# Optimization experiments

Measured on AMD Instinct MI355X. Metric: run time of the kernel, lower is better.

## Reference

```python
import jax, jax.numpy as jnp
import numpy as np

B, DZ, DY, DX = 2, 200, 200, 100   # batch, voxel grid
N = 200000                          # active input voxels
C_IN, C_MID, C_OUT = 16, 64, 32
K = 27                              # 3x3x3 kernel offsets
EPS = 1e-5


def _pad_per_k(kid, a_in, a_out, pad_in, pad_out):
    # pack ragged per-offset pair lists into dense [K, Pmax] with dummy padding
    counts = np.bincount(kid, minlength=K)
    P = int(counts.max())
    I = np.full((K, P), pad_in, np.int32)
    O = np.full((K, P), pad_out, np.int32)
    order = np.argsort(kid, kind='stable')
    ks = kid[order]
    starts = np.cumsum(counts) - counts
    pos = np.arange(kid.size) - starts[ks]
    I[ks, pos] = a_in[order]
    O[ks, pos] = a_out[order]
    return I, O


def _build_structure(seed=0):
    # spconv-style indice-pair generation (rulebook) in numpy
    rng = np.random.default_rng(seed)
    lin = rng.choice(B * DZ * DY * DX, size=N, replace=False)
    b, r = np.divmod(lin, DZ * DY * DX)
    z, r = np.divmod(r, DY * DX)
    y, x = np.divmod(r, DX)
    coords = np.stack([b, z, y, x], 1)
    offs = np.stack(np.meshgrid(*[np.arange(3)] * 3, indexing='ij'), -1).reshape(K, 3)
    od = np.array([(DZ - 3) // 2 + 1, (DY - 3) // 2 + 1, (DX - 3) // 2 + 1])
    # stage 1: SparseConv3d k=3 s=2 p=0 -> output site o iff i = 2*o + k
    oc = coords[:, None, 1:] - offs[None]            # (N, 27, 3)
    valid = (oc >= 0).all(-1) & (oc % 2 == 0).all(-1)
    oq = oc // 2
    valid &= (oq < od).all(-1)
    pi, pk = np.nonzero(valid)
    oz, oy, ox = oq[pi, pk, 0], oq[pi, pk, 1], oq[pi, pk, 2]
    olin = ((coords[pi, 0] * od[0] + oz) * od[1] + oy) * od[2] + ox
    uniq, inv = np.unique(olin, return_inverse=True)
    n1 = int(len(uniq))
    p1_in, p1_out = _pad_per_k(pk, pi.astype(np.int32), inv.astype(np.int32), N, n1)
    # stage 2: SubMConv3d k=3 on stage-1 sites (output sites == input sites)
    c1b, r = np.divmod(uniq, od[0] * od[1] * od[2])
    c1z, r = np.divmod(r, od[1] * od[2])
    c1y, c1x = np.divmod(r, od[2])
    coords1 = np.stack([c1b, c1z, c1y, c1x], 1)
    nc = coords1[:, None, 1:] + (offs - 1)[None]     # (n1, 27, 3) neighbor coords
    valid2 = (nc >= 0).all(-1) & (nc < od).all(-1)
    pj, pk2 = np.nonzero(valid2)
    nl = ((coords1[pj, 0] * od[0] + nc[pj, pk2, 0]) * od[1] + nc[pj, pk2, 1]) * od[2] + nc[pj, pk2, 2]
    pos = np.minimum(np.searchsorted(uniq, nl), n1 - 1)
    ok = uniq[pos] == nl
    p2_in, p2_out = _pad_per_k(pk2[ok], pos[ok].astype(np.int32), pj[ok].astype(np.int32), n1, n1)
    return p1_in, p1_out, p2_in, p2_out, n1


def _ggs(feats, W, pin, pout, n_out):
    # gather-gemm-scatter sparse conv; pin padded with feats.shape[0], pout with n_out
    fpad = jnp.concatenate([feats, jnp.zeros((1, feats.shape[1]), feats.dtype)], 0)
    out = jnp.zeros((n_out + 1, W.shape[2]), feats.dtype)
    for k in range(W.shape[0]):
        out = out.at[pout[k]].add(fpad[pin[k]] @ W[k])
    return out[:n_out]


def _bn_relu(x, g, b):
    # BatchNorm1d (training-mode batch stats, biased var) + ReLU
    m = x.mean(0)
    v = x.var(0)
    return jax.nn.relu((x - m) * jax.lax.rsqrt(v + EPS) * g + b)


def setup_inputs():
    p1_in, p1_out, p2_in, p2_out, n1 = _build_structure(0)
    key = jax.random.key(0)
    k1, k2, k3, k4 = jax.random.split(key, 4)
    return {
        'feats': jax.random.normal(k1, (N, C_IN), jnp.float32),
        'W1': jax.random.normal(k2, (K, C_IN, C_MID), jnp.float32) * 0.05,
        'gamma1': jnp.ones((C_MID,), jnp.float32),
        'beta1': jnp.zeros((C_MID,), jnp.float32),
        'W2': jax.random.normal(k3, (K, C_MID, C_MID), jnp.float32) * 0.05,
        'gamma2': jnp.ones((C_MID,), jnp.float32),
        'beta2': jnp.zeros((C_MID,), jnp.float32),
        'W3': jax.random.normal(k4, (K, C_MID, C_OUT), jnp.float32) * 0.05,
        'p1_in': jnp.asarray(p1_in), 'p1_out': jnp.asarray(p1_out),
        'p2_in': jnp.asarray(p2_in), 'p2_out': jnp.asarray(p2_out),
        'n1': n1,
    }


def reference(feats, W1, gamma1, beta1, W2, gamma2, beta2, W3, p1_in, p1_out, p2_in, p2_out, n1):
    x = _ggs(feats, W1, p1_in, p1_out, n1)                        # SparseConv3d(Cin,64,3,2)
    x = _bn_relu(x, gamma1, beta1)
    x = _bn_relu(_ggs(x, W2, p2_in, p2_out, n1), gamma2, beta2)   # SubMConv3d(64,64,3)
    return _ggs(x, W3, p1_out, p1_in, N)                          # SparseInverseConv3d: pairs swapped
```

## Files before the change

### kernel.cpp

```cpp
#include <hip/hip_runtime.h>
#include <hip/hip_bf16.h>

typedef __bf16 bf16x8 __attribute__((ext_vector_type(8)));
typedef float f32x4 __attribute__((ext_vector_type(4)));

__device__ __forceinline__ unsigned short f2bf(float x) {
  union { float f; unsigned int u; } v; v.f = x;
  unsigned int r = (v.u + 0x7FFFu + ((v.u >> 16) & 1u)) >> 16;
  return (unsigned short)r;
}
__device__ __forceinline__ float bf2f(unsigned short u) {
  union { unsigned int u; float f; } v; v.u = ((unsigned int)u) << 16;
  return v.f;
}

__global__ void cvt_feats_kernel(const float* __restrict__ f, unsigned short* __restrict__ fb, int n16) {
  int t = blockIdx.x * 256 + threadIdx.x;
  if (t >= n16) return;
  fb[t] = f2bf(f[t]);
}

__global__ void pack_w_kernel(const float* __restrict__ W, unsigned short* __restrict__ Wp,
                              int CI, int CO, int NT, int KK) {
  int t = blockIdx.x * 256 + threadIdx.x;
  int total = 27 * NT * KK * 512;
  if (t >= total) return;
  int j = t & 7, l = (t >> 3) & 63;
  int g = t >> 9;
  int kk = g % KK; g /= KK;
  int nt = g % NT; int k = g / NT;
  int kg = kk * 32 + ((l >> 4) * 8) + j;
  int c = nt * 16 + (l & 15);
  float v = (kg < CI) ? W[((size_t)k * CI + kg) * CO + c] : 0.0f;
  Wp[t] = f2bf(v);
}

__global__ void pack_w_paired_kernel(const float* __restrict__ W, unsigned short* __restrict__ Wp,
                                     int CO, int NT) {
  int t = blockIdx.x * 256 + threadIdx.x;
  int total = 14 * NT * 512;
  if (t >= total) return;
  int j = t & 7, l = (t >> 3) & 63;
  int g = t >> 9;
  int nt = g % NT; int gp = g / NT;
  int kg = ((l >> 4) * 8) + j;
  int k = 2 * gp + (kg >= 16 ? 1 : 0);
  int ci = kg & 15;
  int c = nt * 16 + (l & 15);
  float v = (k <= 26) ? W[((size_t)k * 16 + ci) * CO + c] : 0.0f;
  Wp[t] = f2bf(v);
}

__global__ void build_table_kernel(const int* __restrict__ pin, const int* __restrict__ pout,
                                   int P, int maxo, int* __restrict__ tab,
                                   const int* __restrict__ n_ptr, int n_cap) {
  int p = blockIdx.x * 256 + threadIdx.x;
  if (p >= P) return;
  int k = blockIdx.y;
  int n = n_cap;
  if (n_ptr) { int nv = n_ptr[0]; if (nv < n) n = nv; }
  size_t e = (size_t)k * P + p;
  int o = pout[e];
  if (o < n) tab[(size_t)k * maxo + o] = pin[e];
}

#define LDTAB(KC_, TARR) do {                                                    \
    int _k2 = PAIRED ? (2 * (KC_) + klb) : (KC_);                                \
    int _kc = _k2 > 26 ? 26 : _k2;                                               \
    _Pragma("unroll") for (int _m = 0; _m < MT; ++_m) {                          \
      int _t = tab[(size_t)_kc * maxo + rowm[_m]];                               \
      TARR[_m] = (PAIRED && _k2 > 26) ? -1 : _t;                                 \
    }                                                                            \
  } while (0)

#define ISSUE_A(AB, TARR, D) do {                                                \
    if (SKIP) {                                                                  \
      bool _anyv = (TARR[0] >= 0);                                               \
      _Pragma("unroll") for (int _m = 1; _m < MT; ++_m)                          \
        _anyv = _anyv || (TARR[_m] >= 0);                                        \
      D = (__ballot(_anyv) != 0ull);                                             \
    }                                                                            \
    _Pragma("unroll") for (int _m = 0; _m < MT; ++_m) {                          \
      const unsigned short* _s = Xb + (size_t)(TARR[_m] < 0 ? zrow : TARR[_m]) * ROWS + loff; \
      _Pragma("unroll") for (int kk = 0; kk < KK; ++kk)                          \
        AB[_m][kk] = *reinterpret_cast<const bf16x8*>(_s + kk * 32);             \
    }                                                                            \
  } while (0)

#define STAGE_B2(KB, PB) do {                                                    \
    _Pragma("unroll") for (int _s = 0; _s < 2; ++_s) {                           \
      if ((KB) + _s <= MAXK) {                                                   \
        size_t _kb = (size_t)((KB) + _s) * (size_t)SZ;                           \
        _Pragma("unroll") for (int _j = 0; _j < PER; ++_j) {                     \
          int _c = w * PER + _j;                                                 \
          const unsigned char* _gp = WpB + _kb + (size_t)_c * 1024 + (size_t)l * 16; \
          __builtin_amdgcn_global_load_lds(                                      \
              (const __attribute__((address_space(1))) void*)_gp,                \
              (__attribute__((address_space(3))) void*)((PB) + _s * SZ + _c * 1024), 16, 0, 0); \
        }                                                                        \
      }                                                                          \
    }                                                                            \
  } while (0)

#define STEP_CORE(BCUR, AB, D) do {                                              \
    if (!SKIP || (D)) {                                                          \
      _Pragma("unroll") for (int kk = 0; kk < KK; ++kk)                          \
        _Pragma("unroll") for (int nt = 0; nt < NT; ++nt) {                      \
          bf16x8 b = *reinterpret_cast<const bf16x8*>(&(BCUR)[(nt * KK + kk) * 1024 + l * 16]); \
          _Pragma("unroll") for (int _m = 0; _m < MT; ++_m)                      \
            acc[_m][nt] = __builtin_amdgcn_mfma_f32_16x16x32_bf16(AB[_m][kk], b, acc[_m][nt], 0, 0, 0); \
        }                                                                        \
    }                                                                            \
  } while (0)

#define GROUP_BARRIER(NW) do {                                                   \
    __builtin_amdgcn_sched_barrier(0);                                           \
    asm volatile("s_waitcnt vmcnt(%0)" :: "n"(NW) : "memory");                   \
    __builtin_amdgcn_sched_barrier(0);                                           \
    __builtin_amdgcn_s_barrier();                                                \
  } while (0)

template<int KK, int NT, int MT, bool SKIP, bool PAIRED>
__global__ __launch_bounds__(256, 3) void conv_mfma_kernel(
    const unsigned short* __restrict__ Xb, const unsigned short* __restrict__ Wp,
    const int* __restrict__ tab, int maxo, int zrow,
    const int* __restrict__ n_ptr, int n_cap,
    unsigned short* __restrict__ outb, float* __restrict__ outf) {
  const int CO = NT * 16;
  const int ROWS = PAIRED ? 16 : KK * 32;
  const int RPW = 16 * MT;
  constexpr int PER = (KK * NT) / 4;
  constexpr int SZ = KK * NT * 1024;
  constexpr int NSTEP = PAIRED ? 14 : 27;
  constexpr int MAXK = NSTEP - 1;
  constexpr int ITERS = PAIRED ? 3 : 6;
  constexpr int TAIL = NSTEP - 4 * ITERS;
  constexpr int NWAIT  = 2 * MT * KK + 2 * MT;
  constexpr int NWAIT0 = 4 * MT * KK + 4 * MT;

  __shared__ __align__(16) unsigned char Blds[2][2][SZ];

  int bid = blockIdx.x;
  {
    int nwg = gridDim.x;
    int q = nwg >> 3, r = nwg & 7;
    int xcd = bid & 7, orig = bid >> 3;
    bid = (xcd < r ? xcd * (q + 1) : r * (q + 1) + (xcd - r) * q) + orig;
  }

  int w = threadIdx.x >> 6, l = threadIdx.x & 63;
  int n_rows = n_cap;
  if (n_ptr) { int nv = n_ptr[0]; if (nv < n_rows) n_rows = nv; }
  if (bid * 4 * RPW >= n_rows) return;
  int lr = l & 15, lg = l >> 4;
  int klb = lg >> 1;
  int loff = PAIRED ? (lg & 1) * 8 : lg * 8;
  int wbase = bid * 4 * RPW + w * RPW;

  int rowm[MT];
#pragma unroll
  for (int m = 0; m < MT; ++m) {
    int r = wbase + m * 16 + lr;
    rowm[m] = r < n_rows ? r : (n_rows - 1);
  }

  const unsigned char* WpB = (const unsigned char*)Wp;

  f32x4 acc[MT][NT] = {};
  bf16x8 aA[MT][KK], aB[MT][KK], aC[MT][KK], aD[MT][KK];
  int t0[MT], t1[MT], t2[MT], t3[MT];
  bool dA = true, dB = true, dC = true, dD = true;

  unsigned char* b0 = &Blds[0][0][0];
  unsigned char* b1 = &Blds[1][0][0];

  LDTAB(0, t0); LDTAB(1, t1); LDTAB(2, t2); LDTAB(3, t3);
  asm volatile("s_waitcnt vmcnt(0)" ::: "memory");
  __builtin_amdgcn_sched_barrier(0);
  STAGE_B2(0, b0);
  __builtin_amdgcn_sched_barrier(0);
  ISSUE_A(aA, t0, dA); ISSUE_A(aB, t1, dB);
  ISSUE_A(aC, t2, dC); ISSUE_A(aD, t3, dD);
  LDTAB(4, t0); LDTAB(5, t1); LDTAB(6, t2); LDTAB(7, t3);
  GROUP_BARRIER(NWAIT0);

#pragma unroll 1
  for (int j = 0; j < ITERS; ++j) {
    int kb = 4 * j;
    STAGE_B2(kb + 2, b1);
    __builtin_amdgcn_sched_barrier(0);
    STEP_CORE(b0 + 0,  aA, dA); ISSUE_A(aA, t0, dA); LDTAB(kb + 8, t0);
    STEP_CORE(b0 + SZ, aB, dB); ISSUE_A(aB, t1, dB); LDTAB(kb + 9, t1);
    GROUP_BARRIER(NWAIT);
    STAGE_B2(kb + 4, b0);
    __builtin_amdgcn_sched_barrier(0);
    STEP_CORE(b1 + 0,  aC, dC); ISSUE_A(aC, t2, dC); LDTAB(kb + 10, t2);
    STEP_CORE(b1 + SZ, aD, dD); ISSUE_A(aD, t3, dD); LDTAB(kb + 11, t3);
    GROUP_BARRIER(NWAIT);
  }

  if (TAIL == 3) {
    STAGE_B2(4 * ITERS + 2, b1);
  }
  STEP_CORE(b0 + 0,  aA, dA);
  STEP_CORE(b0 + SZ, aB, dB);
  if (TAIL == 3) {
    __builtin_amdgcn_sched_barrier(0);
    asm volatile("s_waitcnt vmcnt(0)" ::: "memory");
    __builtin_amdgcn_sched_barrier(0);
    __builtin_amdgcn_s_barrier();
    STEP_CORE(b1 + 0, aC, dC);
  }

#pragma unroll
  for (int mt = 0; mt < MT; ++mt) {
    int r0 = wbase + mt * 16 + lg * 4;
#pragma unroll
    for (int rr = 0; rr < 4; ++rr) {
      int row = r0 + rr;
      if (row < n_rows) {
#pragma unroll
        for (int nt = 0; nt < NT; ++nt) {
          size_t off = (size_t)row * CO + nt * 16 + lr;
          if (outf) outf[off] = acc[mt][nt][rr];
          else outb[off] = f2bf(acc[mt][nt][rr]);
        }
      }
    }
  }
}

__global__ void bn_stats_kernel(const unsigned short* __restrict__ xb,
                                const int* __restrict__ n_ptr, int n_cap,
                                float* __restrict__ stats) {
  int c = threadIdx.x & 63, q = threadIdx.x >> 6;
  int n = n_ptr[0]; if (n > n_cap) n = n_cap;
  float s = 0.f, ss = 0.f;
  for (int r = blockIdx.x * 4 + q; r < n; r += gridDim.x * 4) {
    float v = bf2f(xb[(size_t)r * 64 + c]);
    s += v; ss += v * v;
  }
  __shared__ float ls[8][64];
  ls[q][c] = s; ls[4 + q][c] = ss;
  __syncthreads();
  if (q == 0) {
    s = ls[0][c] + ls[1][c] + ls[2][c] + ls[3][c];
    ss = ls[4][c] + ls[5][c] + ls[6][c] + ls[7][c];
    atomicAdd(&stats[c], s);
    atomicAdd(&stats[64 + c], ss);
  }
}

__global__ void bn_apply_kernel(unsigned short* __restrict__ xb,
                                const int* __restrict__ n_ptr, int n_cap,
                                const float* __restrict__ stats,
                                const float* __restrict__ gamma, const float* __restrict__ beta) {
  int c = threadIdx.x & 63, q = threadIdx.x >> 6;
  int n = n_ptr[0]; if (n > n_cap) n = n_cap;
  float inv_n = 1.f / (float)n;
  float m = stats[c] * inv_n;
  float var = stats[64 + c] * inv_n - m * m;
  float sc = gamma[c] * rsqrtf(var + 1e-5f);
  float sh = beta[c] - m * sc;
  for (int r = blockIdx.x * 4 + q; r < n; r += gridDim.x * 4) {
    size_t off = (size_t)r * 64 + c;
    float v = bf2f(xb[off]) * sc + sh;
    xb[off] = f2bf(v > 0.f ? v : 0.f);
  }
}

extern "C" void kernel_launch(void* const* d_in, const int* in_sizes, int n_in,
                              void* d_out, int out_size, void* d_ws, size_t ws_size,
                              hipStream_t stream) {
  const float* feats  = (const float*)d_in[0];
  const float* W1     = (const float*)d_in[1];
  const float* g1     = (const float*)d_in[2];
  const float* b1     = (const float*)d_in[3];
  const float* W2     = (const float*)d_in[4];
  const float* g2     = (const float*)d_in[5];
  const float* b2     = (const float*)d_in[6];
  const float* W3     = (const float*)d_in[7];
  const int* p1_in    = (const int*)d_in[8];
  const int* p1_out   = (const int*)d_in[9];
  const int* p2_in    = (const int*)d_in[10];
  const int* p2_out   = (const int*)d_in[11];
  const int* d_n1     = (const int*)d_in[12];
  float* out = (float*)d_out;

  const int N  = in_sizes[0] / 16;
  const int P1 = in_sizes[8] / 27;
  const int P2 = in_sizes[10] / 27;
  long KP1 = in_sizes[8];
  int n1b = (int)(KP1 < 980100 ? KP1 : 980100);
  int maxo = n1b > N ? n1b : N;

  char* p = (char*)d_ws;
  auto alloc = [&](size_t bytes) -> char* {
    char* r = p; p += (bytes + 255) & ~(size_t)255; return r;
  };
  unsigned short* featsb = (unsigned short*)alloc((size_t)(N + 1) * 16 * 2);
  unsigned short* x1b    = (unsigned short*)alloc((size_t)(n1b + 1) * 64 * 2);
  unsigned short* x2b    = (unsigned short*)alloc((size_t)(n1b + 1) * 64 * 2);
  unsigned short* W1p    = (unsigned short*)alloc((size_t)14 * 4 * 512 * 2);
  unsigned short* W2p    = (unsigned short*)alloc((size_t)27 * 4 * 2 * 512 * 2);
  unsigned short* W3p    = (unsigned short*)alloc((size_t)27 * 2 * 2 * 512 * 2);
  int*   tab   = (int*)alloc((size_t)maxo * 27 * 4);
  float* stats = (float*)alloc(256 * 4);
  if ((size_t)(p - (char*)d_ws) > ws_size) return;

  hipMemsetAsync(featsb + (size_t)N * 16, 0, 16 * 2, stream);
  hipMemsetAsync(x1b + (size_t)n1b * 64, 0, 64 * 2, stream);
  hipMemsetAsync(x2b + (size_t)n1b * 64, 0, 64 * 2, stream);
  hipMemsetAsync(stats, 0, 256 * 4, stream);

  cvt_feats_kernel<<<(N * 16 + 255) / 256, 256, 0, stream>>>(feats, featsb, N * 16);
  pack_w_paired_kernel<<<(14 * 4 * 512 + 255) / 256, 256, 0, stream>>>(W1, W1p, 64, 4);
  pack_w_kernel<<<(27 * 4 * 2 * 512 + 255) / 256, 256, 0, stream>>>(W2, W2p, 64, 64, 4, 2);
  pack_w_kernel<<<(27 * 2 * 2 * 512 + 255) / 256, 256, 0, stream>>>(W3, W3p, 64, 32, 2, 2);

  hipMemsetAsync(tab, 0xFF, (size_t)n1b * 27 * 4, stream);
  build_table_kernel<<<dim3((P1 + 255) / 256, 27), 256, 0, stream>>>(
      p1_in, p1_out, P1, n1b, tab, d_n1, n1b);
  conv_mfma_kernel<1, 4, 2, true, true><<<(n1b + 127) / 128, 256, 0, stream>>>(
      featsb, W1p, tab, n1b, N, d_n1, n1b, x1b, nullptr);
  bn_stats_kernel<<<1024, 256, 0, stream>>>(x1b, d_n1, n1b, stats);
  bn_apply_kernel<<<2048, 256, 0, stream>>>(x1b, d_n1, n1b, stats, g1, b1);

  hipMemsetAsync(tab, 0xFF, (size_t)n1b * 27 * 4, stream);
  build_table_kernel<<<dim3((P2 + 255) / 256, 27), 256, 0, stream>>>(
      p2_in, p2_out, P2, n1b, tab, d_n1, n1b);
  conv_mfma_kernel<2, 4, 2, false, false><<<(n1b + 127) / 128, 256, 0, stream>>>(
      x1b, W2p, tab, n1b, n1b, d_n1, n1b, x2b, nullptr);
  bn_stats_kernel<<<1024, 256, 0, stream>>>(x2b, d_n1, n1b, stats + 128);
  bn_apply_kernel<<<2048, 256, 0, stream>>>(x2b, d_n1, n1b, stats + 128, g2, b2);

  hipMemsetAsync(tab, 0xFF, (size_t)N * 27 * 4, stream);
  build_table_kernel<<<dim3((P1 + 255) / 256, 27), 256, 0, stream>>>(
      p1_out, p1_in, P1, N, tab, nullptr, N);
  conv_mfma_kernel<2, 2, 2, true, false><<<(N + 127) / 128, 256, 0, stream>>>(
      x2b, W3p, tab, N, n1b, nullptr, N, nullptr, out);
}
```

Measured before the change: 641.1 us.

## Sort inverse-conv output rows by parity class to skip empty kernel offsets

For the inverse conv stage, each output voxel is classified by the parity of its single valid offset (or as empty), and rows are bucketed with a histogram, prefix and scatter into a permutation. A new MFMA kernel processes rows in permuted order, so whole waves share the same few active offsets and the wave-level ballot skips MFMA work for the other offsets. This adds three small kernels plus an extra full pass over the 27-entry table, and output writes become scattered.

New measurement: 662.1 us. +3.3%, slower.

```diff
diff --git a/kernel.cpp b/kernel.cpp
--- a/kernel.cpp
+++ b/kernel.cpp
@@ -62,6 +62,115 @@
   size_t e = (size_t)k * P + p;
   int o = pout[e];
   if (o < n) tab[(size_t)k * maxo + o] = pin[e];
+}
+
+
+__global__ void class_hist_kernel(const int* __restrict__ tab, int maxo, int n,
+                                  int* __restrict__ cls, int* __restrict__ hist) {
+  __shared__ int lh[9];
+  if (threadIdx.x < 9) lh[threadIdx.x] = 0;
+  __syncthreads();
+  int i = blockIdx.x * 256 + threadIdx.x;
+  if (i < n) {
+    int c = 8;
+#pragma unroll
+    for (int k = 0; k < 27; ++k) {
+      if (tab[(size_t)k * maxo + i] >= 0) {
+        int kz = k / 9, ky = (k / 3) % 3, kx = k % 3;
+        c = ((kz & 1) << 2) | ((ky & 1) << 1) | (kx & 1);
+      }
+    }
+    cls[i] = c;
+    atomicAdd(&lh[c], 1);
+  }
+  __syncthreads();
+  if (threadIdx.x < 9) atomicAdd(&hist[threadIdx.x], lh[threadIdx.x]);
+}
+
+__global__ void prefix9_kernel(const int* __restrict__ hist, int* __restrict__ cursor) {
+  if (threadIdx.x == 0) {
+    int s = 0;
+    for (int c = 0; c < 9; ++c) { cursor[c] = s; s += hist[c]; }
+  }
+}
+
+__global__ void scatter_kernel(const int* __restrict__ cls, int n,
+                               int* __restrict__ cursor, int* __restrict__ perm) {
+  __shared__ int lh[9], lbase[9];
+  if (threadIdx.x < 9) lh[threadIdx.x] = 0;
+  __syncthreads();
+  int i = blockIdx.x * 256 + threadIdx.x;
+  int c = -1, lrank = 0;
+  if (i < n) { c = cls[i]; lrank = atomicAdd(&lh[c], 1); }
+  __syncthreads();
+  if (threadIdx.x < 9) lbase[threadIdx.x] = atomicAdd(&cursor[threadIdx.x], lh[threadIdx.x]);
+  __syncthreads();
+  if (c >= 0) perm[lbase[c] + lrank] = i;
+}
+
+template<int KK, int NT>
+__global__ __launch_bounds__(256, 4) void conv_sorted_kernel(
+    const unsigned short* __restrict__ Xb, const unsigned short* __restrict__ Wp,
+    const int* __restrict__ tab, int maxo, int zrow,
+    const int* __restrict__ perm, int n_rows, float* __restrict__ outf) {
+  const int CO = NT * 16;
+  const int ROWS = KK * 32;
+  int bid = blockIdx.x;
+  int w = threadIdx.x >> 6, l = threadIdx.x & 63;
+  int wbase = (bid * 4 + w) * 32;
+  if (wbase >= n_rows) return;
+  int lr = l & 15, lg = l >> 4;
+  int sr0 = wbase + lr, sr1 = wbase + 16 + lr;
+  bool ok0 = sr0 < n_rows, ok1 = sr1 < n_rows;
+  int row0 = perm[ok0 ? sr0 : (n_rows - 1)];
+  int row1 = perm[ok1 ? sr1 : (n_rows - 1)];
+
+  f32x4 acc[2][NT] = {};
+
+  int t0 = ok0 ? tab[row0] : -1;
+  int t1 = ok1 ? tab[row1] : -1;
+#pragma unroll 1
+  for (int k = 0; k < 27; ++k) {
+    int u0 = -1, u1 = -1;
+    if (k < 26) {
+      u0 = ok0 ? tab[(size_t)(k + 1) * maxo + row0] : -1;
+      u1 = ok1 ? tab[(size_t)(k + 1) * maxo + row1] : -1;
+    }
+    if (__ballot(t0 >= 0 || t1 >= 0) != 0ull) {
+      const unsigned short* s0 = Xb + (size_t)(t0 < 0 ? zrow : t0) * ROWS + lg * 8;
+      const unsigned short* s1 = Xb + (size_t)(t1 < 0 ? zrow : t1) * ROWS + lg * 8;
+      bf16x8 a0[KK], a1[KK];
+#pragma unroll
+      for (int kk = 0; kk < KK; ++kk) {
+        a0[kk] = *reinterpret_cast<const bf16x8*>(s0 + kk * 32);
+        a1[kk] = *reinterpret_cast<const bf16x8*>(s1 + kk * 32);
+      }
+#pragma unroll
+      for (int kk = 0; kk < KK; ++kk)
+#pragma unroll
+        for (int nt = 0; nt < NT; ++nt) {
+          bf16x8 b = *reinterpret_cast<const bf16x8*>(
+              Wp + ((((size_t)k * NT + nt) * KK + kk) << 9) + l * 8);
+          acc[0][nt] = __builtin_amdgcn_mfma_f32_16x16x32_bf16(a0[kk], b, acc[0][nt], 0, 0, 0);
+          acc[1][nt] = __builtin_amdgcn_mfma_f32_16x16x32_bf16(a1[kk], b, acc[1][nt], 0, 0, 0);
+        }
+    }
+    t0 = u0; t1 = u1;
+  }
+
+#pragma unroll
+  for (int mt = 0; mt < 2; ++mt) {
+#pragma unroll
+    for (int rr = 0; rr < 4; ++rr) {
+      int sr = wbase + mt * 16 + lg * 4 + rr;
+      if (sr < n_rows) {
+        int row = perm[sr];
+#pragma unroll
+        for (int nt = 0; nt < NT; ++nt)
+          outf[(size_t)row * CO + nt * 16 + lr] = acc[mt][nt][rr];
+      }
+    }
+  }
 }
 
 #define LDTAB(KC_, TARR) do {                                                    \
@@ -306,12 +415,16 @@
   unsigned short* W3p    = (unsigned short*)alloc((size_t)27 * 2 * 2 * 512 * 2);
   int*   tab   = (int*)alloc((size_t)maxo * 27 * 4);
   float* stats = (float*)alloc(256 * 4);
+  int*   cls   = (int*)alloc((size_t)N * 4);
+  int*   perm  = (int*)alloc((size_t)N * 4);
+  int*   hist  = (int*)alloc(32 * 4);
   if ((size_t)(p - (char*)d_ws) > ws_size) return;
 
   hipMemsetAsync(featsb + (size_t)N * 16, 0, 16 * 2, stream);
   hipMemsetAsync(x1b + (size_t)n1b * 64, 0, 64 * 2, stream);
   hipMemsetAsync(x2b + (size_t)n1b * 64, 0, 64 * 2, stream);
   hipMemsetAsync(stats, 0, 256 * 4, stream);
+  hipMemsetAsync(hist, 0, 32 * 4, stream);
 
   cvt_feats_kernel<<<(N * 16 + 255) / 256, 256, 0, stream>>>(feats, featsb, N * 16);
   pack_w_paired_kernel<<<(14 * 4 * 512 + 255) / 256, 256, 0, stream>>>(W1, W1p, 64, 4);
@@ -337,6 +450,9 @@
   hipMemsetAsync(tab, 0xFF, (size_t)N * 27 * 4, stream);
   build_table_kernel<<<dim3((P1 + 255) / 256, 27), 256, 0, stream>>>(
       p1_out, p1_in, P1, N, tab, nullptr, N);
-  conv_mfma_kernel<2, 2, 2, true, false><<<(N + 127) / 128, 256, 0, stream>>>(
-      x2b, W3p, tab, N, n1b, nullptr, N, nullptr, out);
-}
+  class_hist_kernel<<<(N + 255) / 256, 256, 0, stream>>>(tab, N, N, cls, hist);
+  prefix9_kernel<<<1, 64, 0, stream>>>(hist, hist + 9);
+  scatter_kernel<<<(N + 255) / 256, 256, 0, stream>>>(cls, N, hist + 9, perm);
+  conv_sorted_kernel<2, 2><<<(N + 127) / 128, 256, 0, stream>>>(
+      x2b, W3p, tab, N, n1b, perm, N, out);
+}
```
